# Kernel optimization log

Hardware: AMD Instinct MI355X
Metric: run time of the kernel (lower is better)

## Reference

```python
import jax, jax.numpy as jnp
import numpy as np

B, L, D, A = 4, 4096, 256, 64  # batch, seq_len, n_embd, att_size

def setup_inputs() -> dict:
    key = jax.random.key(0)
    kx, kq, kk, kv = jax.random.split(key, 4)
    x = jax.random.normal(kx, (B, L, D), dtype=jnp.float32)
    # torch nn.Linear(n_embd, att_size) weight is [att_size, n_embd]; we store transposed [D, A]
    s = 1.0 / np.sqrt(D)
    Wq = jax.random.normal(kq, (D, A), dtype=jnp.float32) * s
    Wk = jax.random.normal(kk, (D, A), dtype=jnp.float32) * s
    Wv = jax.random.normal(kv, (D, A), dtype=jnp.float32) * s
    return {"x": x, "Wq": Wq, "Wk": Wk, "Wv": Wv}

def reference(x, Wq, Wk, Wv):
    # q,k,v: [B,L,A]
    q = jnp.einsum('bld,da->bla', x, Wq)
    k = jnp.einsum('bld,da->bla', x, Wk)
    v = jnp.einsum('bld,da->bla', x, Wv)
    # NOTE: original module does NOT scale by 1/sqrt(att_size)
    scores = jnp.einsum('bqa,bka->bqk', q, k)  # [B,L,L]
    Lq = x.shape[1]
    causal = jnp.tril(jnp.ones((Lq, Lq), dtype=bool))
    scores = jnp.where(causal, scores, -jnp.inf)
    weights = jax.nn.softmax(scores, axis=-1)
    # dropout is identity in eval mode
    out = jnp.einsum('bqk,bka->bqa', weights, v)  # [B,L,A]
    return out
```

## Files before the change

kernel.cpp:

```cpp
#include <hip/hip_runtime.h>
#include <math.h>

#define B_ 4
#define L_ 4096
#define D_ 256
#define A_ 64
#define M_ (B_*L_)

typedef _Float16 half4 __attribute__((ext_vector_type(4)));
typedef _Float16 half8 __attribute__((ext_vector_type(8)));
typedef __attribute__((ext_vector_type(4))) float floatx4;

__device__ __forceinline__ unsigned short f2h_(float f) {
    _Float16 h = (_Float16)f;
    return __builtin_bit_cast(unsigned short, h);
}

__global__ __launch_bounds__(256) void wconv_kernel(
    const float* __restrict__ Wq, const float* __restrict__ Wk,
    const float* __restrict__ Wv, unsigned short* __restrict__ wt)
{
    const int w = blockIdx.x, t = threadIdx.x;
    const float* W = (w == 0) ? Wq : (w == 1) ? Wk : Wv;
    unsigned short* o = wt + w * A_ * D_;
    const float scale = (w == 0) ? 1.44269504f : 1.0f;
    __shared__ float T[A_ * 260];
    #pragma unroll
    for (int p = 0; p < 16; ++p) {
        int idx = p * 256 + t;
        int d = idx >> 4, a4 = (idx & 15) * 4;
        float4 v = *(const float4*)(W + d * A_ + a4);
        T[(a4 + 0) * 260 + d] = v.x * scale;
        T[(a4 + 1) * 260 + d] = v.y * scale;
        T[(a4 + 2) * 260 + d] = v.z * scale;
        T[(a4 + 3) * 260 + d] = v.w * scale;
    }
    __syncthreads();
    const int a = t >> 2, d0 = (t & 3) * 64;
    #pragma unroll
    for (int i = 0; i < 16; ++i) {
        float4 v = *(const float4*)(&T[a * 260 + d0 + 4 * i]);
        ushort4 s;
        s.x = f2h_(v.x); s.y = f2h_(v.y); s.z = f2h_(v.z); s.w = f2h_(v.w);
        *(ushort4*)(o + a * D_ + d0 + 4 * i) = s;
    }
}

__global__ __launch_bounds__(384) void proj_kernel(
    const float* __restrict__ x,
    const unsigned short* __restrict__ wt,
    unsigned short* __restrict__ qo,
    unsigned short* __restrict__ ko,
    unsigned short* __restrict__ vto)
{
    __shared__ __align__(16) unsigned short Xh[32 * 264];
    __shared__ __align__(16) unsigned short Cst[6 * 1536];
    const int t = threadIdx.x, m0 = blockIdx.x * 32;

    #pragma unroll
    for (int p = 0; p < 6; ++p) {
        int idx = p * 384 + t;
        if (idx < 2048) {
            int row = idx >> 6, col = (idx & 63) * 4;
            float4 v = *(const float4*)(x + (size_t)(m0 + row) * D_ + col);
            ushort4 s;
            s.x = f2h_(v.x); s.y = f2h_(v.y); s.z = f2h_(v.z); s.w = f2h_(v.w);
            *(ushort4*)(Xh + row * 264 + col) = s;
        }
    }
    __syncthreads();

    const int wid = t >> 6, lane = t & 63, c = lane & 15, g = lane >> 4;
    const int w = wid >> 1, mt = wid & 1;

    half8 xa[8];
    #pragma unroll
    for (int s = 0; s < 8; ++s)
        xa[s] = *(const half8*)(Xh + (16 * mt + c) * 264 + 32 * s + 8 * g);

    const unsigned short* wsrc = wt + w * A_ * D_;
    unsigned short* Cw = Cst + wid * 1536;
    #pragma unroll
    for (int nt = 0; nt < 4; ++nt) {
        floatx4 acc = {0.f, 0.f, 0.f, 0.f};
        #pragma unroll
        for (int s = 0; s < 8; ++s) {
            half8 wb = *(const half8*)(wsrc + (16 * nt + c) * D_ + 32 * s + 8 * g);
            acc = __builtin_amdgcn_mfma_f32_16x16x32_f16(xa[s], wb, acc, 0, 0, 0);
        }
        if (w < 2) {
            #pragma unroll
            for (int r = 0; r < 4; ++r)
                Cw[(4 * g + r) * 72 + 16 * nt + c] = f2h_(acc[r]);
        } else {
            #pragma unroll
            for (int r = 0; r < 4; ++r)
                Cw[(16 * nt + c) * 24 + 4 * g + r] = f2h_(acc[r]);
        }
    }

    if (w < 2) {
        unsigned short* o = (w == 0) ? qo : ko;
        const int row16 = lane >> 2, seg = lane & 3;
        uint4 d0 = *(const uint4*)(Cw + row16 * 72 + seg * 16);
        uint4 d1 = *(const uint4*)(Cw + row16 * 72 + seg * 16 + 8);
        unsigned short* p = o + (size_t)(m0 + 16 * mt + row16) * A_ + seg * 16;
        *(uint4*)(p) = d0;
        *(uint4*)(p + 8) = d1;
    }
    __syncthreads();
    if (t < 256) {
        const int a = t >> 2, quarter = t & 3;
        const int o = quarter * 8, mtv = o >> 4, idx = o & 15;
        uint4 d = *(const uint4*)(Cst + (4 + mtv) * 1536 + a * 24 + idx);
        const int bb = m0 >> 12, l0 = m0 & (L_ - 1);
        *(uint4*)(vto + ((size_t)(bb * A_ + a)) * L_ + l0 + o) = d;
    }
}

__global__ __launch_bounds__(512, 4) void attn_kernel(
    const unsigned short* __restrict__ qb,
    const unsigned short* __restrict__ kb,
    const unsigned short* __restrict__ vt,
    float* __restrict__ poB,
    float2* __restrict__ mlB)
{
    __shared__ __align__(16) unsigned short smem[4 * 4608];
    unsigned short* Ks = smem;
    unsigned short* Vs = smem + 2 * 4608;

    const int t    = threadIdx.x;
    const int lane = t & 63;
    const int wid  = t >> 6;
    const int qsub = wid >> 1;
    const int ph   = wid & 1;
    const int c    = lane & 15;
    const int g    = lane >> 4;

    const int bx = blockIdx.x;
    const int x  = bx & 7, u = bx >> 3;
    const int b  = x >> 1;
    const int gch = 143 - (2 * u + (x & 1));
    int m = 0;
    while (2 * (m + 1) * (m + 2) <= gch) ++m;
    const int rem = gch - 2 * m * (m + 1);
    const int nch = m + 1;
    const int qt  = 4 * m + rem / nch;
    const int j   = rem % nch;
    const int T   = 2 * qt + 2;
    const int t0  = (j * T) / nch;
    const int t1  = ((j + 1) * T) / nch;
    const int nIt = (t1 - t0 + 1) >> 1;
    const int Tm2 = T - 2;

    const int q0    = qt * 128;
    const int qrow0 = q0 + 32 * qsub;
    const int qme0  = qrow0 + c;

    const size_t base  = (size_t)b * L_ * A_;
    const size_t vbase = (size_t)b * A_ * L_;

    half8 qf[2][2];
    #pragma unroll
    for (int f = 0; f < 2; ++f) {
        const unsigned short* qp = qb + base + (size_t)(qrow0 + 16 * f + c) * A_ + g * 8;
        qf[f][0] = *(const half8*)(qp);
        qf[f][1] = *(const half8*)(qp + 32);
    }

    floatx4 O4[2][4];
    #pragma unroll
    for (int f = 0; f < 2; ++f)
        #pragma unroll
        for (int at = 0; at < 4; ++at) O4[f][at] = (floatx4){0.f, 0.f, 0.f, 0.f};
    float m_[2] = {-INFINITY, -INFINITY};
    float l_[2] = {0.f, 0.f};

    for (int it = 0; it < nIt; ++it) {
        __syncthreads();
        #pragma unroll
        for (int tile = 0; tile < 2; ++tile) {
            const int kts = t0 + 2 * it + tile;
            if (kts < t1) {
                const int k0s = kts << 6;
                const int row = t >> 3, c8 = t & 7;
                uint4 dK = *(const uint4*)(kb + base + (size_t)k0s * 64 + t * 8);
                *(uint4*)(Ks + tile * 4608 + row * 72 + c8 * 8) = dK;
                uint4 dV = *(const uint4*)(vt + vbase + (size_t)row * L_ + k0s + c8 * 8);
                *(uint4*)(Vs + tile * 4608 + row * 72 + c8 * 8) = dV;
            }
        }
        __syncthreads();

        const int kt = t0 + 2 * it + ph;
        if (kt >= t1) continue;
        const int k0 = kt << 6;
        const unsigned short* Kw = Ks + ph * 4608;
        const unsigned short* Vw = Vs + ph * 4608;

        half4 pf[2][4];
        #pragma unroll
        for (int f = 0; f < 2; ++f) {
            floatx4 S4[4];
            #pragma unroll
            for (int nt = 0; nt < 4; ++nt) S4[nt] = (floatx4){0.f, 0.f, 0.f, 0.f};
            #pragma unroll
            for (int s = 0; s < 2; ++s)
                #pragma unroll
                for (int nt = 0; nt < 4; ++nt) {
                    half8 kf = *(const half8*)(Kw + (16 * nt + c) * 72 + 32 * s + 8 * g);
                    S4[nt] = __builtin_amdgcn_mfma_f32_16x16x32_f16(kf, qf[f][s], S4[nt], 0, 0, 0);
                }

            if (kt >= Tm2) {
                const int qme = qme0 + 16 * f;
                #pragma unroll
                for (int nt = 0; nt < 4; ++nt)
                    #pragma unroll
                    for (int r = 0; r < 4; ++r)
                        if (k0 + 16 * nt + 4 * g + r > qme) S4[nt][r] = -INFINITY;
            }

            float tm = fmaxf(fmaxf(fmaxf(S4[0][0], S4[0][1]), fmaxf(S4[0][2], S4[0][3])),
                             fmaxf(fmaxf(S4[1][0], S4[1][1]), fmaxf(S4[1][2], S4[1][3])));
            tm = fmaxf(tm, fmaxf(fmaxf(fmaxf(S4[2][0], S4[2][1]), fmaxf(S4[2][2], S4[2][3])),
                                 fmaxf(fmaxf(S4[3][0], S4[3][1]), fmaxf(S4[3][2], S4[3][3]))));
            tm = fmaxf(tm, __shfl_xor(tm, 16));
            tm = fmaxf(tm, __shfl_xor(tm, 32));
            const float mn  = fmaxf(m_[f], tm);
            const float mnc = fmaxf(mn, -3.0e38f);
            const float al  = exp2f(fminf(m_[f] - mnc, 0.f));
            float rs = 0.f;
            #pragma unroll
            for (int nt = 0; nt < 4; ++nt) {
                #pragma unroll
                for (int r = 0; r < 4; ++r) {
                    float p = exp2f(S4[nt][r] - mnc);
                    S4[nt][r] = p;
                    rs += p;
                }
                pf[f][nt][0] = (_Float16)S4[nt][0];
                pf[f][nt][1] = (_Float16)S4[nt][1];
                pf[f][nt][2] = (_Float16)S4[nt][2];
                pf[f][nt][3] = (_Float16)S4[nt][3];
            }
            rs += __shfl_xor(rs, 16);
            rs += __shfl_xor(rs, 32);
            l_[f] = l_[f] * al + rs;
            m_[f] = mn;
            #pragma unroll
            for (int at = 0; at < 4; ++at) O4[f][at] *= al;
        }

        #pragma unroll
        for (int at = 0; at < 4; ++at) {
            #pragma unroll
            for (int nt = 0; nt < 4; ++nt) {
                half4 va = *(const half4*)(Vw + (16 * at + c) * 72 + 16 * nt + 4 * g);
                O4[0][at] = __builtin_amdgcn_mfma_f32_16x16x16f16(va, pf[0][nt], O4[0][at], 0, 0, 0);
                O4[1][at] = __builtin_amdgcn_mfma_f32_16x16x16f16(va, pf[1][nt], O4[1][at], 0, 0, 0);
            }
        }
    }

    float*  Of  = (float*)smem;
    float2* mlb = (float2*)(smem + 16384);
    #pragma unroll
    for (int f = 0; f < 2; ++f) {
        __syncthreads();
        #pragma unroll
        for (int at = 0; at < 4; ++at) {
            float4 v; v.x = O4[f][at][0]; v.y = O4[f][at][1];
            v.z = O4[f][at][2]; v.w = O4[f][at][3];
            ((float4*)Of)[wid * 256 + at * 64 + lane] = v;
        }
        if (g == 0) { float2 ml; ml.x = m_[f]; ml.y = l_[f]; mlb[wid * 16 + c] = ml; }
        __syncthreads();

        const int q64 = t >> 3, seg = t & 7;
        const int qs = q64 >> 4, cc = q64 & 15;
        const int rowq = 32 * qs + 16 * f + cc;
        const float2 A0 = mlb[(2 * qs) * 16 + cc];
        const float2 A1 = mlb[(2 * qs + 1) * 16 + cc];
        const float mf = fmaxf(A0.x, A1.x);
        const float mc = fmaxf(mf, -3.0e38f);
        const float w0 = exp2f(A0.x - mc);
        const float w1 = exp2f(A1.x - mc);
        const float ls = w0 * A0.y + w1 * A1.y;
        float res[8];
        #pragma unroll
        for (int u2 = 0; u2 < 8; ++u2) {
            const int a = seg * 8 + u2;
            const int at = a >> 4, gg = (a >> 2) & 3, r = a & 3;
            const int i0 = ((2 * qs) * 256 + at * 64 + gg * 16 + cc) * 4 + r;
            const int i1 = ((2 * qs + 1) * 256 + at * 64 + gg * 16 + cc) * 4 + r;
            res[u2] = w0 * Of[i0] + w1 * Of[i1];
        }
        float* p = poB + (size_t)j * M_ * A_ + base + (size_t)(q0 + rowq) * A_ + seg * 8;
        *(float4*)(p)     = make_float4(res[0], res[1], res[2], res[3]);
        *(float4*)(p + 4) = make_float4(res[4], res[5], res[6], res[7]);
        if (seg == 0) {
            float2 ml; ml.x = mf; ml.y = ls;
            mlB[(size_t)j * M_ + b * L_ + q0 + rowq] = ml;
        }
    }
}

__global__ __launch_bounds__(256) void merge_kernel(
    float* __restrict__ out, const float* __restrict__ poB,
    const float2* __restrict__ mlB)
{
    const int tg = blockIdx.x * 256 + threadIdx.x;
    const int q = tg >> 4;
    const int qt = (q & (L_ - 1)) >> 7;
    const int nch = (qt + 4) >> 2;
    float mf = -INFINITY, den = 0.f;
    float4 acc = make_float4(0.f, 0.f, 0.f, 0.f);
    #pragma unroll
    for (int jj = 0; jj < 8; ++jj) {
        if (jj < nch) {
            const float2 aj = mlB[(size_t)jj * M_ + q];
            const float mn = fmaxf(mf, aj.x);
            const float mc = fmaxf(mn, -3.0e38f);
            const float sc = exp2f(fminf(mf - mc, 0.f));
            const float wj = exp2f(aj.x - mc);
            const float4 o = ((const float4*)(poB + (size_t)jj * M_ * A_))[tg];
            acc.x = acc.x * sc + o.x * wj;
            acc.y = acc.y * sc + o.y * wj;
            acc.z = acc.z * sc + o.z * wj;
            acc.w = acc.w * sc + o.w * wj;
            den = den * sc + aj.y * wj;
            mf = mn;
        }
    }
    const float inv = 1.f / den;
    float4 r;
    r.x = acc.x * inv; r.y = acc.y * inv; r.z = acc.z * inv; r.w = acc.w * inv;
    ((float4*)out)[tg] = r;
}

extern "C" void kernel_launch(void* const* d_in, const int* in_sizes, int n_in,
                              void* d_out, int out_size, void* d_ws, size_t ws_size,
                              hipStream_t stream) {
    const float* x  = (const float*)d_in[0];
    const float* Wq = (const float*)d_in[1];
    const float* Wk = (const float*)d_in[2];
    const float* Wv = (const float*)d_in[3];

    char* ws = (char*)d_ws;
    unsigned short* qb = (unsigned short*)(ws);
    unsigned short* kb = (unsigned short*)(ws + (2u << 20));
    unsigned short* vt = (unsigned short*)(ws + (4u << 20));
    unsigned short* wt = (unsigned short*)(ws + (6u << 20));
    char* p0 = ws + (6u << 20) + (128u << 10);
    float*  poB = (float*)(p0);
    float2* mlB = (float2*)(p0 + (32u << 20));
    float* out = (float*)d_out;

    hipLaunchKernelGGL(wconv_kernel, dim3(3), dim3(256), 0, stream, Wq, Wk, Wv, wt);
    hipLaunchKernelGGL(proj_kernel, dim3(M_ / 32), dim3(384), 0, stream, x, wt, qb, kb, vt);
    hipLaunchKernelGGL(attn_kernel, dim3(576), dim3(512), 0, stream,
                       qb, kb, vt, poB, mlB);
    hipLaunchKernelGGL(merge_kernel, dim3(1024), dim3(256), 0, stream,
                       out, poB, mlB);
}
```

Measured before the change: 123.6 us.

## Double-buffer K/V tiles with async global-to-LDS loads and XOR swizzle

Loads of K/V tiles now go straight from global memory into LDS via global_load_lds, and the next pair of tiles is prefetched into a second buffer while the current pair is computed. This removes one barrier per iteration and hides global-load latency behind compute. Row padding in LDS is replaced by an XOR swizzle so bank conflicts stay low, and the MFMA sections are wrapped in s_setprio. LDS use grows to 64KB per block, which can cut how many blocks fit on each CU.

```diff
diff --git a/kernel.cpp b/kernel.cpp
--- a/kernel.cpp
+++ b/kernel.cpp
@@ -14,6 +14,12 @@
 __device__ __forceinline__ unsigned short f2h_(float f) {
     _Float16 h = (_Float16)f;
     return __builtin_bit_cast(unsigned short, h);
+}
+
+__device__ __forceinline__ void gll16(const unsigned short* g, unsigned short* l) {
+    __builtin_amdgcn_global_load_lds(
+        (const __attribute__((address_space(1))) unsigned int*)g,
+        (__attribute__((address_space(3))) unsigned int*)l, 16, 0, 0);
 }
 
 __global__ __launch_bounds__(256) void wconv_kernel(
@@ -125,9 +131,9 @@
     float* __restrict__ poB,
     float2* __restrict__ mlB)
 {
-    __shared__ __align__(16) unsigned short smem[4 * 4608];
+    __shared__ __align__(16) unsigned short smem[32768];
     unsigned short* Ks = smem;
-    unsigned short* Vs = smem + 2 * 4608;
+    unsigned short* Vs = smem + 16384;
 
     const int t    = threadIdx.x;
     const int lane = t & 63;
@@ -136,6 +142,10 @@
     const int ph   = wid & 1;
     const int c    = lane & 15;
     const int g    = lane >> 4;
+    const int csw  = (c & 7) * 8;
+
+    const int srow = t >> 3, sc8 = t & 7;
+    const int ssw  = (sc8 ^ (srow & 7)) * 8;
 
     const int bx = blockIdx.x;
     const int x  = bx & 7, u = bx >> 3;
@@ -176,92 +186,106 @@
     float m_[2] = {-INFINITY, -INFINITY};
     float l_[2] = {0.f, 0.f};
 
+    #define STAGE_KV(kts_, slot_) do {                                          \
+        const int k0s_ = (kts_) << 6;                                           \
+        gll16(kb + base + (size_t)(k0s_ + srow) * 64 + ssw,                     \
+              Ks + (slot_) * 4096 + t * 8);                                     \
+        gll16(vt + vbase + (size_t)srow * L_ + k0s_ + ssw,                      \
+              Vs + (slot_) * 4096 + t * 8);                                     \
+    } while (0)
+
+    STAGE_KV(t0, 0);
+    if (t0 + 1 < t1) STAGE_KV(t0 + 1, 1);
+
+    int cur = 0;
     for (int it = 0; it < nIt; ++it) {
         __syncthreads();
-        #pragma unroll
-        for (int tile = 0; tile < 2; ++tile) {
-            const int kts = t0 + 2 * it + tile;
-            if (kts < t1) {
-                const int k0s = kts << 6;
-                const int row = t >> 3, c8 = t & 7;
-                uint4 dK = *(const uint4*)(kb + base + (size_t)k0s * 64 + t * 8);
-                *(uint4*)(Ks + tile * 4608 + row * 72 + c8 * 8) = dK;
-                uint4 dV = *(const uint4*)(vt + vbase + (size_t)row * L_ + k0s + c8 * 8);
-                *(uint4*)(Vs + tile * 4608 + row * 72 + c8 * 8) = dV;
+        const int itb = t0 + 2 * it;
+        if (it + 1 < nIt) {
+            const int nb = itb + 2;
+            STAGE_KV(nb, (cur ^ 1) * 2);
+            if (nb + 1 < t1) STAGE_KV(nb + 1, (cur ^ 1) * 2 + 1);
+        }
+
+        const int kt = itb + ph;
+        if (kt < t1) {
+            const int k0 = kt << 6;
+            const unsigned short* Kw = Ks + (cur * 2 + ph) * 4096;
+            const unsigned short* Vw = Vs + (cur * 2 + ph) * 4096;
+
+            half4 pf[2][4];
+            #pragma unroll
+            for (int f = 0; f < 2; ++f) {
+                floatx4 S4[4];
+                #pragma unroll
+                for (int nt = 0; nt < 4; ++nt) S4[nt] = (floatx4){0.f, 0.f, 0.f, 0.f};
+                __builtin_amdgcn_s_setprio(1);
+                #pragma unroll
+                for (int s = 0; s < 2; ++s)
+                    #pragma unroll
+                    for (int nt = 0; nt < 4; ++nt) {
+                        half8 kf = *(const half8*)(Kw + nt * 1024 + c * 64 +
+                                                   ((s * 32 + g * 8) ^ csw));
+                        S4[nt] = __builtin_amdgcn_mfma_f32_16x16x32_f16(kf, qf[f][s], S4[nt], 0, 0, 0);
+                    }
+                __builtin_amdgcn_s_setprio(0);
+
+                if (kt >= Tm2) {
+                    const int qme = qme0 + 16 * f;
+                    #pragma unroll
+                    for (int nt = 0; nt < 4; ++nt)
+                        #pragma unroll
+                        for (int r = 0; r < 4; ++r)
+                            if (k0 + 16 * nt + 4 * g + r > qme) S4[nt][r] = -INFINITY;
+                }
+
+                float tm = fmaxf(fmaxf(fmaxf(S4[0][0], S4[0][1]), fmaxf(S4[0][2], S4[0][3])),
+                                 fmaxf(fmaxf(S4[1][0], S4[1][1]), fmaxf(S4[1][2], S4[1][3])));
+                tm = fmaxf(tm, fmaxf(fmaxf(fmaxf(S4[2][0], S4[2][1]), fmaxf(S4[2][2], S4[2][3])),
+                                     fmaxf(fmaxf(S4[3][0], S4[3][1]), fmaxf(S4[3][2], S4[3][3]))));
+                tm = fmaxf(tm, __shfl_xor(tm, 16));
+                tm = fmaxf(tm, __shfl_xor(tm, 32));
+                const float mn  = fmaxf(m_[f], tm);
+                const float mnc = fmaxf(mn, -3.0e38f);
+                const float al  = exp2f(fminf(m_[f] - mnc, 0.f));
+                float rs = 0.f;
+                #pragma unroll
+                for (int nt = 0; nt < 4; ++nt) {
+                    #pragma unroll
+                    for (int r = 0; r < 4; ++r) {
+                        float p = exp2f(S4[nt][r] - mnc);
+                        S4[nt][r] = p;
+                        rs += p;
+                    }
+                    pf[f][nt][0] = (_Float16)S4[nt][0];
+                    pf[f][nt][1] = (_Float16)S4[nt][1];
+                    pf[f][nt][2] = (_Float16)S4[nt][2];
+                    pf[f][nt][3] = (_Float16)S4[nt][3];
+                }
+                rs += __shfl_xor(rs, 16);
+                rs += __shfl_xor(rs, 32);
+                l_[f] = l_[f] * al + rs;
+                m_[f] = mn;
+                #pragma unroll
+                for (int at = 0; at < 4; ++at) O4[f][at] *= al;
             }
-        }
-        __syncthreads();
-
-        const int kt = t0 + 2 * it + ph;
-        if (kt >= t1) continue;
-        const int k0 = kt << 6;
-        const unsigned short* Kw = Ks + ph * 4608;
-        const unsigned short* Vw = Vs + ph * 4608;
-
-        half4 pf[2][4];
-        #pragma unroll
-        for (int f = 0; f < 2; ++f) {
-            floatx4 S4[4];
+
+            __builtin_amdgcn_s_setprio(1);
             #pragma unroll
-            for (int nt = 0; nt < 4; ++nt) S4[nt] = (floatx4){0.f, 0.f, 0.f, 0.f};
-            #pragma unroll
-            for (int s = 0; s < 2; ++s)
+            for (int at = 0; at < 4; ++at) {
                 #pragma unroll
                 for (int nt = 0; nt < 4; ++nt) {
-                    half8 kf = *(const half8*)(Kw + (16 * nt + c) * 72 + 32 * s + 8 * g);
-                    S4[nt] = __builtin_amdgcn_mfma_f32_16x16x32_f16(kf, qf[f][s], S4[nt], 0, 0, 0);
+                    half4 va = *(const half4*)(Vw + at * 1024 + c * 64 +
+                                               ((nt * 16 + g * 4) ^ csw));
+                    O4[0][at] = __builtin_amdgcn_mfma_f32_16x16x16f16(va, pf[0][nt], O4[0][at], 0, 0, 0);
+                    O4[1][at] = __builtin_amdgcn_mfma_f32_16x16x16f16(va, pf[1][nt], O4[1][at], 0, 0, 0);
                 }
-
-            if (kt >= Tm2) {
-                const int qme = qme0 + 16 * f;
-                #pragma unroll
-                for (int nt = 0; nt < 4; ++nt)
-                    #pragma unroll
-                    for (int r = 0; r < 4; ++r)
-                        if (k0 + 16 * nt + 4 * g + r > qme) S4[nt][r] = -INFINITY;
             }
-
-            float tm = fmaxf(fmaxf(fmaxf(S4[0][0], S4[0][1]), fmaxf(S4[0][2], S4[0][3])),
-                             fmaxf(fmaxf(S4[1][0], S4[1][1]), fmaxf(S4[1][2], S4[1][3])));
-            tm = fmaxf(tm, fmaxf(fmaxf(fmaxf(S4[2][0], S4[2][1]), fmaxf(S4[2][2], S4[2][3])),
-                                 fmaxf(fmaxf(S4[3][0], S4[3][1]), fmaxf(S4[3][2], S4[3][3]))));
-            tm = fmaxf(tm, __shfl_xor(tm, 16));
-            tm = fmaxf(tm, __shfl_xor(tm, 32));
-            const float mn  = fmaxf(m_[f], tm);
-            const float mnc = fmaxf(mn, -3.0e38f);
-            const float al  = exp2f(fminf(m_[f] - mnc, 0.f));
-            float rs = 0.f;
-            #pragma unroll
-            for (int nt = 0; nt < 4; ++nt) {
-                #pragma unroll
-                for (int r = 0; r < 4; ++r) {
-                    float p = exp2f(S4[nt][r] - mnc);
-                    S4[nt][r] = p;
-                    rs += p;
-                }
-                pf[f][nt][0] = (_Float16)S4[nt][0];
-                pf[f][nt][1] = (_Float16)S4[nt][1];
-                pf[f][nt][2] = (_Float16)S4[nt][2];
-                pf[f][nt][3] = (_Float16)S4[nt][3];
-            }
-            rs += __shfl_xor(rs, 16);
-            rs += __shfl_xor(rs, 32);
-            l_[f] = l_[f] * al + rs;
-            m_[f] = mn;
-            #pragma unroll
-            for (int at = 0; at < 4; ++at) O4[f][at] *= al;
-        }
-
-        #pragma unroll
-        for (int at = 0; at < 4; ++at) {
-            #pragma unroll
-            for (int nt = 0; nt < 4; ++nt) {
-                half4 va = *(const half4*)(Vw + (16 * at + c) * 72 + 16 * nt + 4 * g);
-                O4[0][at] = __builtin_amdgcn_mfma_f32_16x16x16f16(va, pf[0][nt], O4[0][at], 0, 0, 0);
-                O4[1][at] = __builtin_amdgcn_mfma_f32_16x16x16f16(va, pf[1][nt], O4[1][at], 0, 0, 0);
-            }
-        }
-    }
+            __builtin_amdgcn_s_setprio(0);
+        }
+        cur ^= 1;
+    }
+    #undef STAGE_KV
 
     float*  Of  = (float*)smem;
     float2* mlb = (float2*)(smem + 16384);
```

Result: no change. 124.4 us (+0.6%).

## Load K/V fragments directly from global memory and skip redundant softmax rescale

Applied to the files above, without the earlier changes.

Removes the shared-memory staging of K and V tiles and the two block-wide barriers per iteration. Each wave now reads its MFMA operands straight from global memory (L2/cache) and walks its own key tiles independently. It also skips the output and sum rescaling when the running max does not change across the wave. The trade-off is more global and cache traffic with less coalesced, strided V reads, in exchange for no barriers and a smaller LDS footprint that may allow higher occupancy.

```diff
diff --git a/kernel.cpp b/kernel.cpp
--- a/kernel.cpp
+++ b/kernel.cpp
@@ -125,9 +125,8 @@
     float* __restrict__ poB,
     float2* __restrict__ mlB)
 {
-    __shared__ __align__(16) unsigned short smem[4 * 4608];
-    unsigned short* Ks = smem;
-    unsigned short* Vs = smem + 2 * 4608;
+    __shared__ __align__(16) float Of[8 * 1024];
+    __shared__ float2 mlb[128];
 
     const int t    = threadIdx.x;
     const int lane = t & 63;
@@ -150,7 +149,6 @@
     const int T   = 2 * qt + 2;
     const int t0  = (j * T) / nch;
     const int t1  = ((j + 1) * T) / nch;
-    const int nIt = (t1 - t0 + 1) >> 1;
     const int Tm2 = T - 2;
 
     const int q0    = qt * 128;
@@ -176,27 +174,10 @@
     float m_[2] = {-INFINITY, -INFINITY};
     float l_[2] = {0.f, 0.f};
 
-    for (int it = 0; it < nIt; ++it) {
-        __syncthreads();
-        #pragma unroll
-        for (int tile = 0; tile < 2; ++tile) {
-            const int kts = t0 + 2 * it + tile;
-            if (kts < t1) {
-                const int k0s = kts << 6;
-                const int row = t >> 3, c8 = t & 7;
-                uint4 dK = *(const uint4*)(kb + base + (size_t)k0s * 64 + t * 8);
-                *(uint4*)(Ks + tile * 4608 + row * 72 + c8 * 8) = dK;
-                uint4 dV = *(const uint4*)(vt + vbase + (size_t)row * L_ + k0s + c8 * 8);
-                *(uint4*)(Vs + tile * 4608 + row * 72 + c8 * 8) = dV;
-            }
-        }
-        __syncthreads();
-
-        const int kt = t0 + 2 * it + ph;
-        if (kt >= t1) continue;
+    for (int kt = t0 + ph; kt < t1; kt += 2) {
+        const unsigned short* Kp = kb + base + (size_t)(kt << 6) * 64;
+        const unsigned short* Vp = vt + vbase + (kt << 6);
         const int k0 = kt << 6;
-        const unsigned short* Kw = Ks + ph * 4608;
-        const unsigned short* Vw = Vs + ph * 4608;
 
         half4 pf[2][4];
         #pragma unroll
@@ -208,7 +189,7 @@
             for (int s = 0; s < 2; ++s)
                 #pragma unroll
                 for (int nt = 0; nt < 4; ++nt) {
-                    half8 kf = *(const half8*)(Kw + (16 * nt + c) * 72 + 32 * s + 8 * g);
+                    half8 kf = *(const half8*)(Kp + (16 * nt + c) * 64 + s * 32 + g * 8);
                     S4[nt] = __builtin_amdgcn_mfma_f32_16x16x32_f16(kf, qf[f][s], S4[nt], 0, 0, 0);
                 }
 
@@ -227,9 +208,19 @@
                                  fmaxf(fmaxf(S4[3][0], S4[3][1]), fmaxf(S4[3][2], S4[3][3]))));
             tm = fmaxf(tm, __shfl_xor(tm, 16));
             tm = fmaxf(tm, __shfl_xor(tm, 32));
-            const float mn  = fmaxf(m_[f], tm);
-            const float mnc = fmaxf(mn, -3.0e38f);
-            const float al  = exp2f(fminf(m_[f] - mnc, 0.f));
+
+            float mnc;
+            if (__all(tm <= m_[f])) {
+                mnc = fmaxf(m_[f], -3.0e38f);
+            } else {
+                const float mn = fmaxf(m_[f], tm);
+                mnc = fmaxf(mn, -3.0e38f);
+                const float al = exp2f(fminf(m_[f] - mnc, 0.f));
+                l_[f] *= al;
+                m_[f] = mn;
+                #pragma unroll
+                for (int at = 0; at < 4; ++at) O4[f][at] *= al;
+            }
             float rs = 0.f;
             #pragma unroll
             for (int nt = 0; nt < 4; ++nt) {
@@ -246,25 +237,20 @@
             }
             rs += __shfl_xor(rs, 16);
             rs += __shfl_xor(rs, 32);
-            l_[f] = l_[f] * al + rs;
-            m_[f] = mn;
-            #pragma unroll
-            for (int at = 0; at < 4; ++at) O4[f][at] *= al;
+            l_[f] += rs;
         }
 
         #pragma unroll
         for (int at = 0; at < 4; ++at) {
             #pragma unroll
             for (int nt = 0; nt < 4; ++nt) {
-                half4 va = *(const half4*)(Vw + (16 * at + c) * 72 + 16 * nt + 4 * g);
+                half4 va = *(const half4*)(Vp + (size_t)(16 * at + c) * L_ + 16 * nt + 4 * g);
                 O4[0][at] = __builtin_amdgcn_mfma_f32_16x16x16f16(va, pf[0][nt], O4[0][at], 0, 0, 0);
                 O4[1][at] = __builtin_amdgcn_mfma_f32_16x16x16f16(va, pf[1][nt], O4[1][at], 0, 0, 0);
             }
         }
     }
 
-    float*  Of  = (float*)smem;
-    float2* mlb = (float2*)(smem + 16384);
     #pragma unroll
     for (int f = 0; f < 2; ++f) {
         __syncthreads();
```

Measured after the change: 218.9 us. +77.2%, slower.
